# Optimization experiments

Measured on AMD Instinct MI355X. Metric: run time of the kernel, lower is better.

Reference implementation:

```python
import jax, jax.numpy as jnp
import numpy as np

NUM_HEAD = 8
HEAD_DIM = 32
MAX_DIST = 128
RATIO = 4  # smooth_embedding_ratio


def setup_inputs() -> dict:
    key = jax.random.key(0)
    ks = jax.random.split(key, 8)
    B, L, C = 4, 2048, 64
    H, D, md = NUM_HEAD, HEAD_DIM, MAX_DIST
    Wsm = (2 * md + 1) // RATIO  # 64

    def g(k, shape, scale=0.05):
        return jax.random.normal(k, shape, dtype=jnp.float32) * scale

    return {
        "x": g(ks[0], (B, L, C), 1.0),
        "Wq": g(ks[1], (C, H * D)),
        "bq": jnp.zeros((H * D,), jnp.float32),
        "Wk": g(ks[2], (C, H * D)),
        "bk": jnp.zeros((H * D,), jnp.float32),
        "Wv": g(ks[3], (C, H)),
        "distance_pe": g(ks[4], (H, D, Wsm, 1)),
        "u_pe": g(ks[5], (H, 1, 1, D)),
        "v_pe": g(ks[6], (H, 1, 1, D)),
    }


def reference(x, Wq, bq, Wk, bk, Wv, distance_pe, u_pe, v_pe):
    H, D, md = NUM_HEAD, HEAD_DIM, MAX_DIST
    W = 2 * md + 1
    B, L, _ = x.shape

    # projections, split into heads: (H, B, L, D)
    q = (x @ Wq + bq).reshape(B, L, H, D).transpose(2, 0, 1, 3)
    k = (x @ Wk + bk).reshape(B, L, H, D).transpose(2, 0, 1, 3)
    v = jax.nn.sigmoid(x @ Wv).transpose(2, 0, 1)  # (H, B, L)

    # Banded (q+u) @ k^T without materializing the full LxL score matrix.
    # TF does matmul + diag_part(k=(-md, md)) + permute + double reverse, which
    # equals att[h,b,n,m] = <q_u[h,b,(L-1-n)-(m-md)], k[h,b,L-1-n]> (0 if OOB).
    q_u = q + u_pe  # (H, B, L, D)
    q_pad = jnp.pad(q_u, ((0, 0), (0, 0), (md, md), (0, 0)))  # zeros match diag_part padding

    def band_at(m):
        # q_pad[j + 2*md - m] == q_u[j - (m - md)] (zero when out of range)
        qs = jax.lax.dynamic_slice_in_dim(q_pad, 2 * md - m, L, axis=2)
        return jnp.einsum('hbld,hbld->hbl', qs, k)

    band = jax.lax.map(band_at, jnp.arange(W))  # (W, H, B, L)
    att = jnp.transpose(band, (1, 2, 3, 0))[:, :, ::-1, :]  # (H, B, L, W)

    # Smoothed distance PE: bilinear upsample width Wsm -> W (TF2 half-pixel centers)
    smooth_pe = jax.image.resize(distance_pe, (H, D, W, 1), method='linear')[..., 0]  # (H, D, W)
    att = att + jnp.einsum('hbld,hdw->hblw', q + v_pe, smooth_pe)

    att = jax.nn.softmax(att * (float(D) ** -0.5), axis=-1)
    att = att * v[..., None]  # sigmoid value gating

    out = att.sum(axis=2)  # global mode: reduce over data_length -> (H, B, W)
    return jnp.transpose(out, (1, 2, 0))  # (B, W, H)
```

## Files before the change

kernel.cpp:

```cpp
#include <hip/hip_runtime.h>
#include <math.h>

#define NH 8
#define HD 32
#define MD 128
#define NW 257
#define NWP 272
#define WSM 64
#define NB 4
#define NL 2048
#define NC 64
#define NHD 256
#define PR 8
#define NPROJ_BLK (NB * NL / PR)
#define SPE_BLK 34
#define SP 40
#define ROWS 128
#define WIN 384
#define SC2 0.2550928063161107f

using bf16x8 = __attribute__((ext_vector_type(8))) short;
using f32x4  = __attribute__((ext_vector_type(4))) float;
using i32x4  = __attribute__((ext_vector_type(4))) int;

__device__ __forceinline__ unsigned short f2bf(float f) {
  unsigned int u = __builtin_bit_cast(unsigned int, f);
  u = (u + 0x7fffu + ((u >> 16) & 1u)) >> 16;
  return (unsigned short)u;
}

__global__ __launch_bounds__(256) void proj_spe_kernel(
    const float* __restrict__ x,
    const float* __restrict__ Wq, const float* __restrict__ bq,
    const float* __restrict__ Wk, const float* __restrict__ bk,
    const float* __restrict__ Wv, const float* __restrict__ dpe,
    const float* __restrict__ u_pe, const float* __restrict__ v_pe,
    unsigned short* __restrict__ qu, unsigned short* __restrict__ qv,
    unsigned short* __restrict__ kb, float* __restrict__ vv,
    unsigned short* __restrict__ spt, float* __restrict__ out) {
  const int t = threadIdx.x;

  if (blockIdx.x >= NPROJ_BLK) {
    const int base = (blockIdx.x - NPROJ_BLK) * 256 + t;
    if (base < NB * NW * NH) out[base] = 0.f;
    for (int idx = base; idx < NH * NWP * HD; idx += SPE_BLK * 256) {
      const int d = idx & 31;
      const int hm = idx >> 5;
      const int m = hm % NWP;
      const int h = hm / NWP;
      float val = 0.f;
      if (m < NW) {
        float tt = (m + 0.5f) * ((float)WSM / (float)NW) - 0.5f;
        tt = fminf(fmaxf(tt, 0.f), (float)(WSM - 1));
        const int i0 = (int)tt;
        const float f = tt - (float)i0;
        const int i1 = (i0 + 1 < WSM) ? i0 + 1 : WSM - 1;
        const float* bse = dpe + ((size_t)h * HD + d) * WSM;
        val = (bse[i0] * (1.f - f) + bse[i1] * f) * SC2;
      }
      spt[idx] = f2bf(val);
    }
    return;
  }

  __shared__ float xs[PR][NC];
  const int row0 = blockIdx.x * PR;
  if (t < PR * NC / 4)
    reinterpret_cast<float4*>(xs)[t] = reinterpret_cast<const float4*>(x + (size_t)row0 * NC)[t];
  __syncthreads();

  const int h = t >> 5, d = t & 31;
  const float uu = u_pe[t];
  const float vp = v_pe[t];
  float accq[PR], acck[PR];
  const float bq_t = bq[t], bk_t = bk[t];
#pragma unroll
  for (int r = 0; r < PR; ++r) { accq[r] = bq_t; acck[r] = bk_t; }
#pragma unroll
  for (int c4 = 0; c4 < NC / 4; ++c4) {
    float wq4[4], wk4[4];
#pragma unroll
    for (int j = 0; j < 4; ++j) {
      wq4[j] = Wq[(4 * c4 + j) * NHD + t];
      wk4[j] = Wk[(4 * c4 + j) * NHD + t];
    }
#pragma unroll
    for (int r = 0; r < PR; ++r) {
      const float4 xv = *reinterpret_cast<const float4*>(&xs[r][4 * c4]);
      accq[r] = fmaf(xv.x, wq4[0], accq[r]);
      accq[r] = fmaf(xv.y, wq4[1], accq[r]);
      accq[r] = fmaf(xv.z, wq4[2], accq[r]);
      accq[r] = fmaf(xv.w, wq4[3], accq[r]);
      acck[r] = fmaf(xv.x, wk4[0], acck[r]);
      acck[r] = fmaf(xv.y, wk4[1], acck[r]);
      acck[r] = fmaf(xv.z, wk4[2], acck[r]);
      acck[r] = fmaf(xv.w, wk4[3], acck[r]);
    }
  }
#pragma unroll
  for (int r = 0; r < PR; ++r) {
    const int row = row0 + r;
    const int b = row >> 11, l = row & (NL - 1);
    const size_t o = (((size_t)h * NB + b) * NL + l) * HD + d;
    qu[o] = f2bf(accq[r] + uu);
    qv[o] = f2bf(accq[r] + vp);
    kb[o] = f2bf(acck[r] * SC2);
  }
  if (t < PR * NH) {
    const int r = t >> 3, hh = t & 7;
    float a = 0.f;
#pragma unroll
    for (int c4 = 0; c4 < NC / 4; ++c4) {
      const float4 xv = *reinterpret_cast<const float4*>(&xs[r][4 * c4]);
      a = fmaf(xv.x, Wv[(4 * c4 + 0) * NH + hh], a);
      a = fmaf(xv.y, Wv[(4 * c4 + 1) * NH + hh], a);
      a = fmaf(xv.z, Wv[(4 * c4 + 2) * NH + hh], a);
      a = fmaf(xv.w, Wv[(4 * c4 + 3) * NH + hh], a);
    }
    const int row = row0 + r;
    const int b = row >> 11, l = row & (NL - 1);
    vv[((size_t)hh * NB + b) * NL + l] = 1.f / (1.f + __expf(-a));
  }
}

__global__ __launch_bounds__(512, 4) void band_attn_mfma(
    const unsigned short* __restrict__ qu, const unsigned short* __restrict__ qv,
    const unsigned short* __restrict__ kb, const float* __restrict__ vv,
    const unsigned short* __restrict__ spt, float* __restrict__ out) {
  __shared__ __align__(16) unsigned short qu_sh[WIN * SP];
  float* red = reinterpret_cast<float*>(qu_sh);

  const int bid = blockIdx.x;
  const int tile = bid & 15;
  const int hb = bid >> 4;
  const int b = hb & (NB - 1);
  const int h = hb >> 2;
  const int n0 = tile << 7;
  const int jlo = NL - ROWS - n0;
  const int tid = threadIdx.x;
  const int l = tid & 63;
  const int w = tid >> 6;
  const int c = l & 15;
  const int g = l >> 4;
  const int g8 = g * 8;

  const unsigned short* qu_h = qu + (size_t)hb * NL * HD;
  const unsigned short* qv_h = qv + (size_t)hb * NL * HD;
  const unsigned short* k_h  = kb + (size_t)hb * NL * HD;
  const unsigned short* sp_h = spt + (size_t)h * NWP * HD;
  const float* vv_h = vv + (size_t)hb * NL;

  const bf16x8 ak  = *reinterpret_cast<const bf16x8*>(k_h  + (size_t)(jlo + 16 * w + c) * HD + g8);
  const bf16x8 aqv = *reinterpret_cast<const bf16x8*>(qv_h + (size_t)(n0 + 127 - 16 * w - c) * HD + g8);
  const f32x4 v4 = *reinterpret_cast<const f32x4*>(vv_h + (n0 + 124 - 16 * w - 4 * g));

  const int wq0_blk = jlo - MD;
  i32x4 stq[3];
#pragma unroll
  for (int it = 0; it < 3; ++it) {
    const int p = tid + it * 512;
    const int gr = wq0_blk + (p >> 2);
    i32x4 val = {0, 0, 0, 0};
    if ((unsigned)gr < (unsigned)NL)
      val = *reinterpret_cast<const i32x4*>(qu_h + (size_t)gr * HD + (p & 3) * 8);
    stq[it] = val;
  }

  const f32x4 z4 = {0.f, 0.f, 0.f, 0.f};

  f32x4 s[17];
#pragma unroll
  for (int t = 0; t < 17; ++t) {
    const bf16x8 bsp = *reinterpret_cast<const bf16x8*>(sp_h + (size_t)(16 * t + c) * HD + g8);
    s[t] = __builtin_amdgcn_mfma_f32_16x16x32_bf16(aqv, bsp, z4, 0, 0, 0);
  }

#pragma unroll
  for (int it = 0; it < 3; ++it) {
    const int p = tid + it * 512;
    *reinterpret_cast<i32x4*>(&qu_sh[(p >> 2) * SP + (p & 3) * 8]) = stq[it];
  }
  __syncthreads();

  int sl[4]; bool cond[4];
#pragma unroll
  for (int r = 0; r < 4; ++r) {
    sl[r] = 16 * g + ((4 * g + r - c) & 15);
    cond[r] = (4 * g + r) >= c;
  }

  f32x4 shp;
#pragma unroll
  for (int U = 0; U <= 16; ++U) {
    const bf16x8 bqu = *reinterpret_cast<const bf16x8*>(&qu_sh[(16 * w + 16 * U + c) * SP + g8]);
    const f32x4 c1 = __builtin_amdgcn_mfma_f32_16x16x32_bf16(ak, bqu, z4, 0, 0, 0);

    f32x4 shc;
#pragma unroll
    for (int r = 0; r < 4; ++r) shc[r] = __shfl(c1[r], sl[r], 64);

    if (U == 0) {
#pragma unroll
      for (int r = 0; r < 4; ++r)
        s[16][r] = (c == 0) ? (s[16][r] + shc[r]) : -1e30f;
    } else {
#pragma unroll
      for (int r = 0; r < 4; ++r)
        s[16 - U][r] += cond[r] ? shc[r] : shp[r];
    }
    shp = shc;
  }

  float wgt[4];
#pragma unroll
  for (int r = 0; r < 4; ++r) {
    float sum = 0.f;
#pragma unroll
    for (int t = 0; t < 17; ++t) {
      const float p = exp2f(s[t][r]);
      s[t][r] = p;
      sum += p;
    }
#pragma unroll
    for (int off = 1; off < 16; off <<= 1) sum += __shfl_xor(sum, off, 16);
    wgt[r] = v4[3 - r] * __builtin_amdgcn_rcpf(sum);
  }

  __syncthreads();
#pragma unroll
  for (int t = 0; t < 17; ++t) {
    float y = s[t][0] * wgt[0] + s[t][1] * wgt[1] + s[t][2] * wgt[2] + s[t][3] * wgt[3];
    y += __shfl_xor(y, 16, 64);
    y += __shfl_xor(y, 32, 64);
    if (l < 16) red[w * NWP + 16 * t + c] = y;
  }
  __syncthreads();
  for (int m = tid; m < NW; m += 512) {
    float ssum = 0.f;
#pragma unroll
    for (int ww = 0; ww < 8; ++ww) ssum += red[ww * NWP + m];
    atomicAdd(&out[((size_t)b * NW + m) * NH + h], ssum);
  }
}

extern "C" void kernel_launch(void* const* d_in, const int* in_sizes, int n_in,
                              void* d_out, int out_size, void* d_ws, size_t ws_size,
                              hipStream_t stream) {
  const float* x = (const float*)d_in[0];
  const float* Wq = (const float*)d_in[1];
  const float* bq = (const float*)d_in[2];
  const float* Wk = (const float*)d_in[3];
  const float* bk = (const float*)d_in[4];
  const float* Wv = (const float*)d_in[5];
  const float* dpe = (const float*)d_in[6];
  const float* u_pe = (const float*)d_in[7];
  const float* v_pe = (const float*)d_in[8];
  float* out = (float*)d_out;

  const size_t qk_elems = (size_t)NH * NB * NL * HD;
  float* vv = (float*)d_ws;
  unsigned short* qu = (unsigned short*)(vv + (size_t)NH * NB * NL);
  unsigned short* qv = qu + qk_elems;
  unsigned short* kb = qv + qk_elems;
  unsigned short* spt = kb + qk_elems;

  hipLaunchKernelGGL(proj_spe_kernel, dim3(NPROJ_BLK + SPE_BLK), dim3(256), 0, stream,
                     x, Wq, bq, Wk, bk, Wv, dpe, u_pe, v_pe, qu, qv, kb, vv, spt, out);
  hipLaunchKernelGGL(band_attn_mfma, dim3(NH * NB * (NL / ROWS)), dim3(512), 0, stream,
                     qu, qv, kb, vv, spt, out);
}
```

Baseline: 38.69 us.

## Use MFMA for Q/K projection and enlarge band-attention tiles to 256 rows

Rewrites the projection stage as a bf16 MFMA matmul with per-warp 16-row tiles. It splits the sigmoid value-gate projection into separate blocks and switches bf16 conversion to the hardware pack instruction. The band attention kernel now runs 1024-thread blocks over 256-row tiles, so the shared q window is amortized over more rows and fewer atomics are issued per output. The risks are lower occupancy from the larger blocks, uncoalesced strided weight loads in the projection, and bf16 rounding of x and the weights.

Result: faster. 36.90 us (-4.6%).

```diff
diff --git a/kernel.cpp b/kernel.cpp
--- a/kernel.cpp
+++ b/kernel.cpp
@@ -11,25 +11,29 @@
 #define NL 2048
 #define NC 64
 #define NHD 256
-#define PR 8
-#define NPROJ_BLK (NB * NL / PR)
+#define SP 40
+#define ROWS 256
+#define WIN 512
+#define SC2 0.2550928063161107f
+
+#define PM_BLK 512
+#define VV_BLK 64
 #define SPE_BLK 34
-#define SP 40
-#define ROWS 128
-#define WIN 384
-#define SC2 0.2550928063161107f
 
 using bf16x8 = __attribute__((ext_vector_type(8))) short;
 using f32x4  = __attribute__((ext_vector_type(4))) float;
 using i32x4  = __attribute__((ext_vector_type(4))) int;
 
-__device__ __forceinline__ unsigned short f2bf(float f) {
-  unsigned int u = __builtin_bit_cast(unsigned int, f);
-  u = (u + 0x7fffu + ((u >> 16) & 1u)) >> 16;
-  return (unsigned short)u;
-}
-
-__global__ __launch_bounds__(256) void proj_spe_kernel(
+__device__ __forceinline__ unsigned cvtpk(float lo, float hi) {
+  unsigned r;
+  asm("v_cvt_pk_bf16_f32 %0, %1, %2" : "=v"(r) : "v"(lo), "v"(hi));
+  return r;
+}
+__device__ __forceinline__ void stb(unsigned short* p, float f) {
+  *p = (unsigned short)cvtpk(f, f);
+}
+
+__global__ __launch_bounds__(256, 4) void projmm_kernel(
     const float* __restrict__ x,
     const float* __restrict__ Wq, const float* __restrict__ bq,
     const float* __restrict__ Wk, const float* __restrict__ bk,
@@ -39,9 +43,10 @@
     unsigned short* __restrict__ kb, float* __restrict__ vv,
     unsigned short* __restrict__ spt, float* __restrict__ out) {
   const int t = threadIdx.x;
-
-  if (blockIdx.x >= NPROJ_BLK) {
-    const int base = (blockIdx.x - NPROJ_BLK) * 256 + t;
+  const int bid = blockIdx.x;
+
+  if (bid >= PM_BLK + VV_BLK) {
+    const int base = (bid - PM_BLK - VV_BLK) * 256 + t;
     if (base < NB * NW * NH) out[base] = 0.f;
     for (int idx = base; idx < NH * NWP * HD; idx += SPE_BLK * 256) {
       const int d = idx & 31;
@@ -58,72 +63,106 @@
         const float* bse = dpe + ((size_t)h * HD + d) * WSM;
         val = (bse[i0] * (1.f - f) + bse[i1] * f) * SC2;
       }
-      spt[idx] = f2bf(val);
+      stb(spt + idx, val);
     }
     return;
   }
 
-  __shared__ float xs[PR][NC];
-  const int row0 = blockIdx.x * PR;
-  if (t < PR * NC / 4)
-    reinterpret_cast<float4*>(xs)[t] = reinterpret_cast<const float4*>(x + (size_t)row0 * NC)[t];
-  __syncthreads();
-
-  const int h = t >> 5, d = t & 31;
-  const float uu = u_pe[t];
-  const float vp = v_pe[t];
-  float accq[PR], acck[PR];
-  const float bq_t = bq[t], bk_t = bk[t];
-#pragma unroll
-  for (int r = 0; r < PR; ++r) { accq[r] = bq_t; acck[r] = bk_t; }
-#pragma unroll
-  for (int c4 = 0; c4 < NC / 4; ++c4) {
-    float wq4[4], wk4[4];
-#pragma unroll
-    for (int j = 0; j < 4; ++j) {
-      wq4[j] = Wq[(4 * c4 + j) * NHD + t];
-      wk4[j] = Wk[(4 * c4 + j) * NHD + t];
-    }
-#pragma unroll
-    for (int r = 0; r < PR; ++r) {
-      const float4 xv = *reinterpret_cast<const float4*>(&xs[r][4 * c4]);
-      accq[r] = fmaf(xv.x, wq4[0], accq[r]);
-      accq[r] = fmaf(xv.y, wq4[1], accq[r]);
-      accq[r] = fmaf(xv.z, wq4[2], accq[r]);
-      accq[r] = fmaf(xv.w, wq4[3], accq[r]);
-      acck[r] = fmaf(xv.x, wk4[0], acck[r]);
-      acck[r] = fmaf(xv.y, wk4[1], acck[r]);
-      acck[r] = fmaf(xv.z, wk4[2], acck[r]);
-      acck[r] = fmaf(xv.w, wk4[3], acck[r]);
-    }
-  }
-#pragma unroll
-  for (int r = 0; r < PR; ++r) {
-    const int row = row0 + r;
-    const int b = row >> 11, l = row & (NL - 1);
-    const size_t o = (((size_t)h * NB + b) * NL + l) * HD + d;
-    qu[o] = f2bf(accq[r] + uu);
-    qv[o] = f2bf(accq[r] + vp);
-    kb[o] = f2bf(acck[r] * SC2);
-  }
-  if (t < PR * NH) {
-    const int r = t >> 3, hh = t & 7;
-    float a = 0.f;
+  if (bid >= PM_BLK) {
+    const int row = (bid - PM_BLK) * 128 + (t >> 1);
+    const int h0 = (t & 1) * 4;
+    const float* xr = x + (size_t)row * NC;
+    float a0 = 0.f, a1 = 0.f, a2 = 0.f, a3 = 0.f;
 #pragma unroll
     for (int c4 = 0; c4 < NC / 4; ++c4) {
-      const float4 xv = *reinterpret_cast<const float4*>(&xs[r][4 * c4]);
-      a = fmaf(xv.x, Wv[(4 * c4 + 0) * NH + hh], a);
-      a = fmaf(xv.y, Wv[(4 * c4 + 1) * NH + hh], a);
-      a = fmaf(xv.z, Wv[(4 * c4 + 2) * NH + hh], a);
-      a = fmaf(xv.w, Wv[(4 * c4 + 3) * NH + hh], a);
-    }
-    const int row = row0 + r;
-    const int b = row >> 11, l = row & (NL - 1);
-    vv[((size_t)hh * NB + b) * NL + l] = 1.f / (1.f + __expf(-a));
-  }
-}
-
-__global__ __launch_bounds__(512, 4) void band_attn_mfma(
+      const float4 xv = *reinterpret_cast<const float4*>(xr + 4 * c4);
+#pragma unroll
+      for (int j = 0; j < 4; ++j) {
+        const float xs = j == 0 ? xv.x : j == 1 ? xv.y : j == 2 ? xv.z : xv.w;
+        const float4 wv = *reinterpret_cast<const float4*>(Wv + (4 * c4 + j) * NH + h0);
+        a0 = fmaf(xs, wv.x, a0);
+        a1 = fmaf(xs, wv.y, a1);
+        a2 = fmaf(xs, wv.z, a2);
+        a3 = fmaf(xs, wv.w, a3);
+      }
+    }
+    const int b = row >> 11, ll = row & (NL - 1);
+    vv[((size_t)(h0 + 0) * NB + b) * NL + ll] = 1.f / (1.f + __expf(-a0));
+    vv[((size_t)(h0 + 1) * NB + b) * NL + ll] = 1.f / (1.f + __expf(-a1));
+    vv[((size_t)(h0 + 2) * NB + b) * NL + ll] = 1.f / (1.f + __expf(-a2));
+    vv[((size_t)(h0 + 3) * NB + b) * NL + ll] = 1.f / (1.f + __expf(-a3));
+    return;
+  }
+
+  const int l64 = t & 63, w = t >> 6;
+  const int c = l64 & 15, g = l64 >> 4, g8 = g * 8;
+  const int br = bid >> 2;
+  const int c0 = (bid & 3) << 7;
+  const int r0 = br << 6;
+  const int b = r0 >> 11;
+  const int l0 = r0 & (NL - 1);
+
+  const float* xr = x + (size_t)(r0 + 16 * w + c) * NC;
+  const float4 x00 = *reinterpret_cast<const float4*>(xr + g8);
+  const float4 x01 = *reinterpret_cast<const float4*>(xr + g8 + 4);
+  const float4 x10 = *reinterpret_cast<const float4*>(xr + 32 + g8);
+  const float4 x11 = *reinterpret_cast<const float4*>(xr + 32 + g8 + 4);
+  const i32x4 a0i = {(int)cvtpk(x00.x, x00.y), (int)cvtpk(x00.z, x00.w),
+                     (int)cvtpk(x01.x, x01.y), (int)cvtpk(x01.z, x01.w)};
+  const i32x4 a1i = {(int)cvtpk(x10.x, x10.y), (int)cvtpk(x10.z, x10.w),
+                     (int)cvtpk(x11.x, x11.y), (int)cvtpk(x11.z, x11.w)};
+  const bf16x8 a0 = __builtin_bit_cast(bf16x8, a0i);
+  const bf16x8 a1 = __builtin_bit_cast(bf16x8, a1i);
+
+  const bool isQ = (c0 < 256);
+  const float* Wsrc = isQ ? Wq : Wk;
+  const int cb = isQ ? c0 : c0 - 256;
+
+  f32x4 acc[8];
+#pragma unroll
+  for (int tt = 0; tt < 8; ++tt) acc[tt] = {0.f, 0.f, 0.f, 0.f};
+
+#pragma unroll
+  for (int tt = 0; tt < 8; ++tt) {
+    const float* wp = Wsrc + cb + 16 * tt + c;
+    float f0[8], f1[8];
+#pragma unroll
+    for (int j = 0; j < 8; ++j) {
+      f0[j] = wp[(g8 + j) * NHD];
+      f1[j] = wp[(32 + g8 + j) * NHD];
+    }
+    const i32x4 b0i = {(int)cvtpk(f0[0], f0[1]), (int)cvtpk(f0[2], f0[3]),
+                       (int)cvtpk(f0[4], f0[5]), (int)cvtpk(f0[6], f0[7])};
+    const i32x4 b1i = {(int)cvtpk(f1[0], f1[1]), (int)cvtpk(f1[2], f1[3]),
+                       (int)cvtpk(f1[4], f1[5]), (int)cvtpk(f1[6], f1[7])};
+    acc[tt] = __builtin_amdgcn_mfma_f32_16x16x32_bf16(a0, __builtin_bit_cast(bf16x8, b0i), acc[tt], 0, 0, 0);
+    acc[tt] = __builtin_amdgcn_mfma_f32_16x16x32_bf16(a1, __builtin_bit_cast(bf16x8, b1i), acc[tt], 0, 0, 0);
+  }
+
+#pragma unroll
+  for (int tt = 0; tt < 8; ++tt) {
+    const int col = cb + 16 * tt + c;
+    const int h = col >> 5, d = col & 31;
+    const size_t rowbase = (((size_t)h * NB + b) * NL + l0 + 16 * w) * HD + d;
+    if (isQ) {
+      const float bias = bq[col];
+      const float uu = u_pe[col], vp = v_pe[col];
+#pragma unroll
+      for (int r = 0; r < 4; ++r) {
+        const float val = acc[tt][r] + bias;
+        stb(qu + rowbase + (size_t)(4 * g + r) * HD, val + uu);
+        stb(qv + rowbase + (size_t)(4 * g + r) * HD, val + vp);
+      }
+    } else {
+      const float bias = bk[col];
+#pragma unroll
+      for (int r = 0; r < 4; ++r)
+        stb(kb + rowbase + (size_t)(4 * g + r) * HD, (acc[tt][r] + bias) * SC2);
+    }
+  }
+}
+
+__global__ __launch_bounds__(1024, 4) void band_attn_mfma(
     const unsigned short* __restrict__ qu, const unsigned short* __restrict__ qv,
     const unsigned short* __restrict__ kb, const float* __restrict__ vv,
     const unsigned short* __restrict__ spt, float* __restrict__ out) {
@@ -131,11 +170,11 @@
   float* red = reinterpret_cast<float*>(qu_sh);
 
   const int bid = blockIdx.x;
-  const int tile = bid & 15;
-  const int hb = bid >> 4;
+  const int tile = bid & 7;
+  const int hb = bid >> 3;
   const int b = hb & (NB - 1);
   const int h = hb >> 2;
-  const int n0 = tile << 7;
+  const int n0 = tile << 8;
   const int jlo = NL - ROWS - n0;
   const int tid = threadIdx.x;
   const int l = tid & 63;
@@ -151,14 +190,14 @@
   const float* vv_h = vv + (size_t)hb * NL;
 
   const bf16x8 ak  = *reinterpret_cast<const bf16x8*>(k_h  + (size_t)(jlo + 16 * w + c) * HD + g8);
-  const bf16x8 aqv = *reinterpret_cast<const bf16x8*>(qv_h + (size_t)(n0 + 127 - 16 * w - c) * HD + g8);
-  const f32x4 v4 = *reinterpret_cast<const f32x4*>(vv_h + (n0 + 124 - 16 * w - 4 * g));
+  const bf16x8 aqv = *reinterpret_cast<const bf16x8*>(qv_h + (size_t)(n0 + 255 - 16 * w - c) * HD + g8);
+  const f32x4 v4 = *reinterpret_cast<const f32x4*>(vv_h + (n0 + 252 - 16 * w - 4 * g));
 
   const int wq0_blk = jlo - MD;
-  i32x4 stq[3];
-#pragma unroll
-  for (int it = 0; it < 3; ++it) {
-    const int p = tid + it * 512;
+  i32x4 stq[2];
+#pragma unroll
+  for (int it = 0; it < 2; ++it) {
+    const int p = tid + it * 1024;
     const int gr = wq0_blk + (p >> 2);
     i32x4 val = {0, 0, 0, 0};
     if ((unsigned)gr < (unsigned)NL)
@@ -176,8 +215,8 @@
   }
 
 #pragma unroll
-  for (int it = 0; it < 3; ++it) {
-    const int p = tid + it * 512;
+  for (int it = 0; it < 2; ++it) {
+    const int p = tid + it * 1024;
     *reinterpret_cast<i32x4*>(&qu_sh[(p >> 2) * SP + (p & 3) * 8]) = stq[it];
   }
   __syncthreads();
@@ -235,10 +274,10 @@
     if (l < 16) red[w * NWP + 16 * t + c] = y;
   }
   __syncthreads();
-  for (int m = tid; m < NW; m += 512) {
+  for (int m = tid; m < NW; m += 1024) {
     float ssum = 0.f;
 #pragma unroll
-    for (int ww = 0; ww < 8; ++ww) ssum += red[ww * NWP + m];
+    for (int ww = 0; ww < 16; ++ww) ssum += red[ww * NWP + m];
     atomicAdd(&out[((size_t)b * NW + m) * NH + h], ssum);
   }
 }
@@ -264,8 +303,8 @@
   unsigned short* kb = qv + qk_elems;
   unsigned short* spt = kb + qk_elems;
 
-  hipLaunchKernelGGL(proj_spe_kernel, dim3(NPROJ_BLK + SPE_BLK), dim3(256), 0, stream,
+  hipLaunchKernelGGL(projmm_kernel, dim3(PM_BLK + VV_BLK + SPE_BLK), dim3(256), 0, stream,
                      x, Wq, bq, Wk, bk, Wv, dpe, u_pe, v_pe, qu, qv, kb, vv, spt, out);
-  hipLaunchKernelGGL(band_attn_mfma, dim3(NH * NB * (NL / ROWS)), dim3(512), 0, stream,
+  hipLaunchKernelGGL(band_attn_mfma, dim3(NH * NB * (NL / ROWS)), dim3(1024), 0, stream,
                      qu, qv, kb, vv, spt, out);
 }
```

## Fuse QKV projection and smoothed PE into band attention kernel using MFMA

Applied to the files above, without the earlier changes.

Removes the separate projection kernel and its global bf16 q/k intermediates. Each attention block now computes its own q_u window, k, q_v and sigmoid gate from x with bf16 MFMAs on LDS-staged weight tiles. It also rebuilds the interpolated distance PE in LDS. Output zeroing moves to a memset. The aim is to cut global memory traffic and a kernel launch, at the cost of redundant projection work for overlapping q windows (384 rows per 128-row tile) and bf16 rounding of x and weights.

Measured after the change: 44.80 us. 1.16x slower.

```diff
diff --git a/kernel.cpp b/kernel.cpp
--- a/kernel.cpp
+++ b/kernel.cpp
@@ -11,132 +11,64 @@
 #define NL 2048
 #define NC 64
 #define NHD 256
-#define PR 8
-#define NPROJ_BLK (NB * NL / PR)
-#define SPE_BLK 34
-#define SP 40
 #define ROWS 128
 #define WIN 384
+#define SPQ 40
 #define SC2 0.2550928063161107f
+
+#define QU_OFF 0
+#define KT_OFF (WIN * SPQ)
+#define QVT_OFF (KT_OFF + ROWS * HD)
+#define WT_OFF (QVT_OFF + ROWS * HD)
+#define SMEM_N (WT_OFF + 2 * 32 * 72)
+#define SP_OFF KT_OFF
 
 using bf16x8 = __attribute__((ext_vector_type(8))) short;
 using f32x4  = __attribute__((ext_vector_type(4))) float;
 using i32x4  = __attribute__((ext_vector_type(4))) int;
 
-__device__ __forceinline__ unsigned short f2bf(float f) {
-  unsigned int u = __builtin_bit_cast(unsigned int, f);
-  u = (u + 0x7fffu + ((u >> 16) & 1u)) >> 16;
-  return (unsigned short)u;
-}
-
-__global__ __launch_bounds__(256) void proj_spe_kernel(
+__device__ __forceinline__ unsigned cvtpk(float lo, float hi) {
+  unsigned r;
+  asm("v_cvt_pk_bf16_f32 %0, %1, %2" : "=v"(r) : "v"(lo), "v"(hi));
+  return r;
+}
+
+__device__ __forceinline__ void ldx_frag(const float* xrow, bool ok, int g8,
+                                         bf16x8* A0, bf16x8* A1) {
+  float4 x00 = {0.f, 0.f, 0.f, 0.f}, x01 = x00, x10 = x00, x11 = x00;
+  if (ok) {
+    x00 = *reinterpret_cast<const float4*>(xrow + g8);
+    x01 = *reinterpret_cast<const float4*>(xrow + g8 + 4);
+    x10 = *reinterpret_cast<const float4*>(xrow + 32 + g8);
+    x11 = *reinterpret_cast<const float4*>(xrow + 32 + g8 + 4);
+  }
+  const i32x4 a0i = {(int)cvtpk(x00.x, x00.y), (int)cvtpk(x00.z, x00.w),
+                     (int)cvtpk(x01.x, x01.y), (int)cvtpk(x01.z, x01.w)};
+  const i32x4 a1i = {(int)cvtpk(x10.x, x10.y), (int)cvtpk(x10.z, x10.w),
+                     (int)cvtpk(x11.x, x11.y), (int)cvtpk(x11.z, x11.w)};
+  *A0 = __builtin_bit_cast(bf16x8, a0i);
+  *A1 = __builtin_bit_cast(bf16x8, a1i);
+}
+
+__global__ __launch_bounds__(512, 4) void fused_kernel(
     const float* __restrict__ x,
     const float* __restrict__ Wq, const float* __restrict__ bq,
     const float* __restrict__ Wk, const float* __restrict__ bk,
     const float* __restrict__ Wv, const float* __restrict__ dpe,
     const float* __restrict__ u_pe, const float* __restrict__ v_pe,
-    unsigned short* __restrict__ qu, unsigned short* __restrict__ qv,
-    unsigned short* __restrict__ kb, float* __restrict__ vv,
-    unsigned short* __restrict__ spt, float* __restrict__ out) {
-  const int t = threadIdx.x;
-
-  if (blockIdx.x >= NPROJ_BLK) {
-    const int base = (blockIdx.x - NPROJ_BLK) * 256 + t;
-    if (base < NB * NW * NH) out[base] = 0.f;
-    for (int idx = base; idx < NH * NWP * HD; idx += SPE_BLK * 256) {
-      const int d = idx & 31;
-      const int hm = idx >> 5;
-      const int m = hm % NWP;
-      const int h = hm / NWP;
-      float val = 0.f;
-      if (m < NW) {
-        float tt = (m + 0.5f) * ((float)WSM / (float)NW) - 0.5f;
-        tt = fminf(fmaxf(tt, 0.f), (float)(WSM - 1));
-        const int i0 = (int)tt;
-        const float f = tt - (float)i0;
-        const int i1 = (i0 + 1 < WSM) ? i0 + 1 : WSM - 1;
-        const float* bse = dpe + ((size_t)h * HD + d) * WSM;
-        val = (bse[i0] * (1.f - f) + bse[i1] * f) * SC2;
-      }
-      spt[idx] = f2bf(val);
-    }
-    return;
-  }
-
-  __shared__ float xs[PR][NC];
-  const int row0 = blockIdx.x * PR;
-  if (t < PR * NC / 4)
-    reinterpret_cast<float4*>(xs)[t] = reinterpret_cast<const float4*>(x + (size_t)row0 * NC)[t];
-  __syncthreads();
-
-  const int h = t >> 5, d = t & 31;
-  const float uu = u_pe[t];
-  const float vp = v_pe[t];
-  float accq[PR], acck[PR];
-  const float bq_t = bq[t], bk_t = bk[t];
-#pragma unroll
-  for (int r = 0; r < PR; ++r) { accq[r] = bq_t; acck[r] = bk_t; }
-#pragma unroll
-  for (int c4 = 0; c4 < NC / 4; ++c4) {
-    float wq4[4], wk4[4];
-#pragma unroll
-    for (int j = 0; j < 4; ++j) {
-      wq4[j] = Wq[(4 * c4 + j) * NHD + t];
-      wk4[j] = Wk[(4 * c4 + j) * NHD + t];
-    }
-#pragma unroll
-    for (int r = 0; r < PR; ++r) {
-      const float4 xv = *reinterpret_cast<const float4*>(&xs[r][4 * c4]);
-      accq[r] = fmaf(xv.x, wq4[0], accq[r]);
-      accq[r] = fmaf(xv.y, wq4[1], accq[r]);
-      accq[r] = fmaf(xv.z, wq4[2], accq[r]);
-      accq[r] = fmaf(xv.w, wq4[3], accq[r]);
-      acck[r] = fmaf(xv.x, wk4[0], acck[r]);
-      acck[r] = fmaf(xv.y, wk4[1], acck[r]);
-      acck[r] = fmaf(xv.z, wk4[2], acck[r]);
-      acck[r] = fmaf(xv.w, wk4[3], acck[r]);
-    }
-  }
-#pragma unroll
-  for (int r = 0; r < PR; ++r) {
-    const int row = row0 + r;
-    const int b = row >> 11, l = row & (NL - 1);
-    const size_t o = (((size_t)h * NB + b) * NL + l) * HD + d;
-    qu[o] = f2bf(accq[r] + uu);
-    qv[o] = f2bf(accq[r] + vp);
-    kb[o] = f2bf(acck[r] * SC2);
-  }
-  if (t < PR * NH) {
-    const int r = t >> 3, hh = t & 7;
-    float a = 0.f;
-#pragma unroll
-    for (int c4 = 0; c4 < NC / 4; ++c4) {
-      const float4 xv = *reinterpret_cast<const float4*>(&xs[r][4 * c4]);
-      a = fmaf(xv.x, Wv[(4 * c4 + 0) * NH + hh], a);
-      a = fmaf(xv.y, Wv[(4 * c4 + 1) * NH + hh], a);
-      a = fmaf(xv.z, Wv[(4 * c4 + 2) * NH + hh], a);
-      a = fmaf(xv.w, Wv[(4 * c4 + 3) * NH + hh], a);
-    }
-    const int row = row0 + r;
-    const int b = row >> 11, l = row & (NL - 1);
-    vv[((size_t)hh * NB + b) * NL + l] = 1.f / (1.f + __expf(-a));
-  }
-}
-
-__global__ __launch_bounds__(512, 4) void band_attn_mfma(
-    const unsigned short* __restrict__ qu, const unsigned short* __restrict__ qv,
-    const unsigned short* __restrict__ kb, const float* __restrict__ vv,
-    const unsigned short* __restrict__ spt, float* __restrict__ out) {
-  __shared__ __align__(16) unsigned short qu_sh[WIN * SP];
-  float* red = reinterpret_cast<float*>(qu_sh);
+    float* __restrict__ out) {
+  __shared__ __align__(16) unsigned short lds[SMEM_N];
+  __shared__ __align__(16) float vvl[ROWS];
 
   const int bid = blockIdx.x;
   const int tile = bid & 15;
   const int hb = bid >> 4;
   const int b = hb & (NB - 1);
   const int h = hb >> 2;
+  const int hc0 = h * HD;
   const int n0 = tile << 7;
   const int jlo = NL - ROWS - n0;
+  const int wq0 = jlo - MD;
   const int tid = threadIdx.x;
   const int l = tid & 63;
   const int w = tid >> 6;
@@ -144,43 +76,148 @@
   const int g = l >> 4;
   const int g8 = g * 8;
 
-  const unsigned short* qu_h = qu + (size_t)hb * NL * HD;
-  const unsigned short* qv_h = qv + (size_t)hb * NL * HD;
-  const unsigned short* k_h  = kb + (size_t)hb * NL * HD;
-  const unsigned short* sp_h = spt + (size_t)h * NWP * HD;
-  const float* vv_h = vv + (size_t)hb * NL;
-
-  const bf16x8 ak  = *reinterpret_cast<const bf16x8*>(k_h  + (size_t)(jlo + 16 * w + c) * HD + g8);
-  const bf16x8 aqv = *reinterpret_cast<const bf16x8*>(qv_h + (size_t)(n0 + 127 - 16 * w - c) * HD + g8);
-  const f32x4 v4 = *reinterpret_cast<const f32x4*>(vv_h + (n0 + 124 - 16 * w - 4 * g));
-
-  const int wq0_blk = jlo - MD;
-  i32x4 stq[3];
-#pragma unroll
-  for (int it = 0; it < 3; ++it) {
-    const int p = tid + it * 512;
-    const int gr = wq0_blk + (p >> 2);
-    i32x4 val = {0, 0, 0, 0};
-    if ((unsigned)gr < (unsigned)NL)
-      val = *reinterpret_cast<const i32x4*>(qu_h + (size_t)gr * HD + (p & 3) * 8);
-    stq[it] = val;
+  const float* xb = x + (size_t)b * NL * NC;
+
+#pragma unroll
+  for (int i = 0; i < 4; ++i) {
+    const int flat = tid + i * 512;
+    const int col = flat & 31;
+    const int kp = (flat >> 5) & 31;
+    const int ws = flat >> 10;
+    const float* Wsrc = ws ? Wk : Wq;
+    const float w0 = Wsrc[(2 * kp) * NHD + hc0 + col];
+    const float w1 = Wsrc[(2 * kp + 1) * NHD + hc0 + col];
+    *reinterpret_cast<unsigned*>(&lds[WT_OFF + ((ws * 32 + col) * 72 + 2 * kp)]) = cvtpk(w0, w1);
+  }
+  if (tid < ROWS) {
+    const float* xr = xb + (size_t)(n0 + tid) * NC;
+    float a = 0.f;
+#pragma unroll
+    for (int k4 = 0; k4 < NC / 4; ++k4) {
+      const float4 xv = *reinterpret_cast<const float4*>(xr + 4 * k4);
+      a = fmaf(xv.x, Wv[(4 * k4 + 0) * NH + h], a);
+      a = fmaf(xv.y, Wv[(4 * k4 + 1) * NH + h], a);
+      a = fmaf(xv.z, Wv[(4 * k4 + 2) * NH + h], a);
+      a = fmaf(xv.w, Wv[(4 * k4 + 3) * NH + h], a);
+    }
+    vvl[tid] = 1.f / (1.f + __expf(-a));
+  }
+  __syncthreads();
+
+  bf16x8 bw[2][2][2];
+#pragma unroll
+  for (int ws = 0; ws < 2; ++ws)
+#pragma unroll
+    for (int ct = 0; ct < 2; ++ct)
+#pragma unroll
+      for (int ks = 0; ks < 2; ++ks)
+        bw[ws][ct][ks] = *reinterpret_cast<const bf16x8*>(
+            &lds[WT_OFF + ((ws * 32 + ct * 16 + c) * 72 + ks * 32 + g8)]);
+
+  float biasQU[2], biasQV[2], biasK[2];
+#pragma unroll
+  for (int ct = 0; ct < 2; ++ct) {
+    const int d = ct * 16 + c;
+    const float bqv = bq[hc0 + d];
+    biasQU[ct] = bqv + u_pe[hc0 + d];
+    biasQV[ct] = bqv + v_pe[hc0 + d];
+    biasK[ct] = bk[hc0 + d];
   }
 
   const f32x4 z4 = {0.f, 0.f, 0.f, 0.f};
 
+#pragma unroll
+  for (int rt = 0; rt < 3; ++rt) {
+    const int wr0 = 48 * w + 16 * rt;
+    const int gr = wq0 + wr0 + c;
+    bf16x8 a0, a1;
+    ldx_frag(xb + (size_t)gr * NC, (unsigned)gr < (unsigned)NL, g8, &a0, &a1);
+    f32x4 acc0 = z4, acc1 = z4;
+    acc0 = __builtin_amdgcn_mfma_f32_16x16x32_bf16(a0, bw[0][0][0], acc0, 0, 0, 0);
+    acc0 = __builtin_amdgcn_mfma_f32_16x16x32_bf16(a1, bw[0][0][1], acc0, 0, 0, 0);
+    acc1 = __builtin_amdgcn_mfma_f32_16x16x32_bf16(a0, bw[0][1][0], acc1, 0, 0, 0);
+    acc1 = __builtin_amdgcn_mfma_f32_16x16x32_bf16(a1, bw[0][1][1], acc1, 0, 0, 0);
+#pragma unroll
+    for (int ct = 0; ct < 2; ++ct) {
+      const f32x4 acc = ct ? acc1 : acc0;
+      const int d = ct * 16 + c;
+#pragma unroll
+      for (int r = 0; r < 4; ++r) {
+        const int wr = wr0 + 4 * g + r;
+        const float val = ((unsigned)(wq0 + wr) < (unsigned)NL) ? acc[r] + biasQU[ct] : 0.f;
+        lds[QU_OFF + wr * SPQ + d] = (unsigned short)cvtpk(val, val);
+      }
+    }
+  }
+  {
+    const int gr = jlo + 16 * w + c;
+    bf16x8 a0, a1;
+    ldx_frag(xb + (size_t)gr * NC, true, g8, &a0, &a1);
+    f32x4 acc0 = z4, acc1 = z4;
+    acc0 = __builtin_amdgcn_mfma_f32_16x16x32_bf16(a0, bw[1][0][0], acc0, 0, 0, 0);
+    acc0 = __builtin_amdgcn_mfma_f32_16x16x32_bf16(a1, bw[1][0][1], acc0, 0, 0, 0);
+    acc1 = __builtin_amdgcn_mfma_f32_16x16x32_bf16(a0, bw[1][1][0], acc1, 0, 0, 0);
+    acc1 = __builtin_amdgcn_mfma_f32_16x16x32_bf16(a1, bw[1][1][1], acc1, 0, 0, 0);
+#pragma unroll
+    for (int ct = 0; ct < 2; ++ct) {
+      const f32x4 acc = ct ? acc1 : acc0;
+#pragma unroll
+      for (int r = 0; r < 4; ++r) {
+        const float val = (acc[r] + biasK[ct]) * SC2;
+        lds[KT_OFF + (16 * w + 4 * g + r) * HD + ct * 16 + c] = (unsigned short)cvtpk(val, val);
+      }
+    }
+  }
+  {
+    const int gr = n0 + 16 * w + c;
+    bf16x8 a0, a1;
+    ldx_frag(xb + (size_t)gr * NC, true, g8, &a0, &a1);
+    f32x4 acc0 = z4, acc1 = z4;
+    acc0 = __builtin_amdgcn_mfma_f32_16x16x32_bf16(a0, bw[0][0][0], acc0, 0, 0, 0);
+    acc0 = __builtin_amdgcn_mfma_f32_16x16x32_bf16(a1, bw[0][0][1], acc0, 0, 0, 0);
+    acc1 = __builtin_amdgcn_mfma_f32_16x16x32_bf16(a0, bw[0][1][0], acc1, 0, 0, 0);
+    acc1 = __builtin_amdgcn_mfma_f32_16x16x32_bf16(a1, bw[0][1][1], acc1, 0, 0, 0);
+#pragma unroll
+    for (int ct = 0; ct < 2; ++ct) {
+      const f32x4 acc = ct ? acc1 : acc0;
+#pragma unroll
+      for (int r = 0; r < 4; ++r) {
+        const float val = acc[r] + biasQV[ct];
+        lds[QVT_OFF + (16 * w + 4 * g + r) * HD + ct * 16 + c] = (unsigned short)cvtpk(val, val);
+      }
+    }
+  }
+  __syncthreads();
+
+  const bf16x8 ak  = *reinterpret_cast<const bf16x8*>(&lds[KT_OFF + (16 * w + c) * HD + g8]);
+  const bf16x8 aqv = *reinterpret_cast<const bf16x8*>(&lds[QVT_OFF + (ROWS - 1 - 16 * w - c) * HD + g8]);
+  const f32x4 v4 = *reinterpret_cast<const f32x4*>(&vvl[ROWS - 4 - 16 * w - 4 * g]);
+  __syncthreads();
+
+#pragma unroll
+  for (int i = 0; i < 17; ++i) {
+    const int idx = tid + i * 512;
+    const int d = idx & 31, m = idx >> 5;
+    float val = 0.f;
+    if (m < NW) {
+      float t2 = (m + 0.5f) * ((float)WSM / (float)NW) - 0.5f;
+      t2 = fminf(fmaxf(t2, 0.f), (float)(WSM - 1));
+      const int i0 = (int)t2;
+      const float f = t2 - (float)i0;
+      const int i1 = (i0 + 1 < WSM) ? i0 + 1 : WSM - 1;
+      const float* bse = dpe + (size_t)(hc0 + d) * WSM;
+      val = (bse[i0] * (1.f - f) + bse[i1] * f) * SC2;
+    }
+    lds[SP_OFF + m * SPQ + d] = (unsigned short)cvtpk(val, val);
+  }
+  __syncthreads();
+
   f32x4 s[17];
 #pragma unroll
   for (int t = 0; t < 17; ++t) {
-    const bf16x8 bsp = *reinterpret_cast<const bf16x8*>(sp_h + (size_t)(16 * t + c) * HD + g8);
+    const bf16x8 bsp = *reinterpret_cast<const bf16x8*>(&lds[SP_OFF + (16 * t + c) * SPQ + g8]);
     s[t] = __builtin_amdgcn_mfma_f32_16x16x32_bf16(aqv, bsp, z4, 0, 0, 0);
   }
-
-#pragma unroll
-  for (int it = 0; it < 3; ++it) {
-    const int p = tid + it * 512;
-    *reinterpret_cast<i32x4*>(&qu_sh[(p >> 2) * SP + (p & 3) * 8]) = stq[it];
-  }
-  __syncthreads();
 
   int sl[4]; bool cond[4];
 #pragma unroll
@@ -192,13 +229,11 @@
   f32x4 shp;
 #pragma unroll
   for (int U = 0; U <= 16; ++U) {
-    const bf16x8 bqu = *reinterpret_cast<const bf16x8*>(&qu_sh[(16 * w + 16 * U + c) * SP + g8]);
+    const bf16x8 bqu = *reinterpret_cast<const bf16x8*>(&lds[QU_OFF + (16 * w + 16 * U + c) * SPQ + g8]);
     const f32x4 c1 = __builtin_amdgcn_mfma_f32_16x16x32_bf16(ak, bqu, z4, 0, 0, 0);
-
     f32x4 shc;
 #pragma unroll
     for (int r = 0; r < 4; ++r) shc[r] = __shfl(c1[r], sl[r], 64);
-
     if (U == 0) {
 #pragma unroll
       for (int r = 0; r < 4; ++r)
@@ -227,6 +262,7 @@
   }
 
   __syncthreads();
+  float* red = reinterpret_cast<float*>(&lds[QU_OFF]);
 #pragma unroll
   for (int t = 0; t < 17; ++t) {
     float y = s[t][0] * wgt[0] + s[t][1] * wgt[1] + s[t][2] * wgt[2] + s[t][3] * wgt[3];
@@ -257,15 +293,7 @@
   const float* v_pe = (const float*)d_in[8];
   float* out = (float*)d_out;
 
-  const size_t qk_elems = (size_t)NH * NB * NL * HD;
-  float* vv = (float*)d_ws;
-  unsigned short* qu = (unsigned short*)(vv + (size_t)NH * NB * NL);
-  unsigned short* qv = qu + qk_elems;
-  unsigned short* kb = qv + qk_elems;
-  unsigned short* spt = kb + qk_elems;
-
-  hipLaunchKernelGGL(proj_spe_kernel, dim3(NPROJ_BLK + SPE_BLK), dim3(256), 0, stream,
-                     x, Wq, bq, Wk, bk, Wv, dpe, u_pe, v_pe, qu, qv, kb, vv, spt, out);
-  hipLaunchKernelGGL(band_attn_mfma, dim3(NH * NB * (NL / ROWS)), dim3(512), 0, stream,
-                     qu, qv, kb, vv, spt, out);
-}
+  hipMemsetAsync(d_out, 0, (size_t)out_size * sizeof(float), stream);
+  hipLaunchKernelGGL(fused_kernel, dim3(NH * NB * (NL / ROWS)), dim3(512), 0, stream,
+                     x, Wq, bq, Wk, bk, Wv, dpe, u_pe, v_pe, out);
+}
```
